# Optimization experiments

Hardware: AMD Instinct MI355X
Metric: run time of the kernel (lower is better)

## Reference

```python
import jax, jax.numpy as jnp
import numpy as np

N_ATOMS = 2_000_000
N_MOL = 50_000
NODE_DIM = 128
HIDDEN_DIM = 64


def setup_inputs() -> dict:
    key = jax.random.key(0)
    k1, k2, k3, k4, k5 = jax.random.split(key, 5)
    x_scalar = jax.random.normal(k1, (N_ATOMS, NODE_DIM), dtype=jnp.float32)
    batch = jnp.sort(jax.random.randint(k2, (N_ATOMS,), 0, N_MOL, dtype=jnp.int32))
    charge = jax.random.normal(k3, (N_MOL,), dtype=jnp.float32)
    W1 = jax.random.normal(k4, (NODE_DIM, HIDDEN_DIM), dtype=jnp.float32) / np.sqrt(NODE_DIM)
    b1 = jnp.zeros((HIDDEN_DIM,), dtype=jnp.float32)  # init.zeros_
    W2 = jax.random.normal(k5, (HIDDEN_DIM, 1), dtype=jnp.float32) / np.sqrt(HIDDEN_DIM)
    b2 = jnp.zeros((1,), dtype=jnp.float32)  # node_bias = 0.0
    return {"x_scalar": x_scalar, "batch": batch, "charge": charge,
            "W1": W1, "b1": b1, "W2": W2, "b2": b2}


def reference(x_scalar, batch, charge, W1, b1, W2, b2):
    # tiny per-atom MLP: 128 -> 64 (silu) -> 1
    h = jax.nn.silu(x_scalar @ W1 + b1)            # [N, 64]
    atom_out = (h @ W2 + b2).squeeze(-1)           # [N]
    n_mol = charge.shape[0]
    # per-molecule reductions keyed by batch
    sum_chrg = jax.ops.segment_sum(atom_out, batch, num_segments=n_mol)          # [B]
    num_atoms = jax.ops.segment_sum(jnp.ones_like(atom_out), batch, num_segments=n_mol)  # [B]
    # gather back per atom and apply total-charge correction
    tot_chrg = charge[batch]                       # [N]
    at_chrgs = atom_out + (tot_chrg - sum_chrg[batch]) / num_atoms[batch]
    return at_chrgs
```

## Files before the change

kernel.cpp:

```cpp
#include <hip/hip_runtime.h>
#include <stdint.h>

typedef __attribute__((ext_vector_type(8))) short bf16x8;
typedef __attribute__((ext_vector_type(4))) float f32x4;

__device__ inline short f2bf(float f) {
    uint32_t u = __builtin_bit_cast(uint32_t, f);
    u += 0x7FFFu + ((u >> 16) & 1u);
    return (short)(u >> 16);
}

__global__ __launch_bounds__(256) void k1_mlp(
        const float* __restrict__ X, const float* __restrict__ W1,
        const float* __restrict__ b1, const float* __restrict__ W2,
        const float* __restrict__ b2, float* __restrict__ out, int N) {
    const int lane = threadIdx.x & 63;
    const int col  = lane & 15;
    const int quad = lane >> 4;
    const int wid   = blockIdx.x * (blockDim.x >> 6) + (threadIdx.x >> 6);
    const int nwave = gridDim.x * (blockDim.x >> 6);

    bf16x8 bfrag[4][4];
#pragma unroll
    for (int nt = 0; nt < 4; ++nt)
#pragma unroll
        for (int s = 0; s < 4; ++s)
#pragma unroll
            for (int j = 0; j < 8; ++j)
                bfrag[nt][s][j] = f2bf(W1[(quad * 8 + j + 32 * s) * 64 + 16 * nt + col]);

    float b1v[4], w2v[4];
#pragma unroll
    for (int nt = 0; nt < 4; ++nt) {
        b1v[nt] = b1[16 * nt + col];
        w2v[nt] = W2[16 * nt + col];
    }
    const float b2v = b2[0];

    const int ntiles = N >> 4;
    for (int tile = wid; tile < ntiles; tile += nwave) {
        const int row0 = tile << 4;
        const float* __restrict__ xrow = X + (size_t)(row0 + col) * 128;

        f32x4 xa[4][2];
#pragma unroll
        for (int s = 0; s < 4; ++s) {
            const float* p = xrow + quad * 8 + 32 * s;
            xa[s][0] = *(const f32x4*)(p);
            xa[s][1] = *(const f32x4*)(p + 4);
        }

        f32x4 acc[4] = {{0.f,0.f,0.f,0.f},{0.f,0.f,0.f,0.f},
                        {0.f,0.f,0.f,0.f},{0.f,0.f,0.f,0.f}};
#pragma unroll
        for (int s = 0; s < 4; ++s) {
            bf16x8 afrag;
#pragma unroll
            for (int j = 0; j < 4; ++j) {
                afrag[j]     = f2bf(xa[s][0][j]);
                afrag[4 + j] = f2bf(xa[s][1][j]);
            }
#pragma unroll
            for (int nt = 0; nt < 4; ++nt)
                acc[nt] = __builtin_amdgcn_mfma_f32_16x16x32_bf16(
                              afrag, bfrag[nt][s], acc[nt], 0, 0, 0);
        }

        float p[4] = {0.f, 0.f, 0.f, 0.f};
#pragma unroll
        for (int nt = 0; nt < 4; ++nt) {
#pragma unroll
            for (int j = 0; j < 4; ++j) {
                float h  = acc[nt][j] + b1v[nt];
                float sg = 1.0f / (1.0f + __expf(-h));
                p[j] += h * sg * w2v[nt];
            }
        }
#pragma unroll
        for (int m = 1; m <= 8; m <<= 1)
#pragma unroll
            for (int j = 0; j < 4; ++j)
                p[j] += __shfl_xor(p[j], m, 64);

        if (col == 0) {
            f32x4 v = {p[0] + b2v, p[1] + b2v, p[2] + b2v, p[3] + b2v};
            *(f32x4*)(out + row0 + quad * 4) = v;
        }
    }
}

__global__ __launch_bounds__(256) void k2_seg(
        const float* __restrict__ atomout, const int* __restrict__ batch,
        const float* __restrict__ charge, float* __restrict__ corr, int N, int B) {
    int m = blockIdx.x * blockDim.x + threadIdx.x;
    if (m >= B) return;
    int lo = 0, hi = N;
    while (lo < hi) { int mid = (lo + hi) >> 1; if (batch[mid] < m) lo = mid + 1; else hi = mid; }
    int start = lo;
    lo = start; hi = N;
    while (lo < hi) { int mid = (lo + hi) >> 1; if (batch[mid] < m + 1) lo = mid + 1; else hi = mid; }
    int end = lo;
    float s = 0.f;
    for (int i = start; i < end; ++i) s += atomout[i];
    int cnt = end - start;
    corr[m] = (cnt > 0) ? (charge[m] - s) / (float)cnt : 0.f;
}

__global__ __launch_bounds__(256) void k3_apply(
        float* __restrict__ out, const int* __restrict__ batch,
        const float* __restrict__ corr, int N) {
    int i = blockIdx.x * blockDim.x + threadIdx.x;
    if (i < N) out[i] += corr[batch[i]];
}

extern "C" void kernel_launch(void* const* d_in, const int* in_sizes, int n_in,
                              void* d_out, int out_size, void* d_ws, size_t ws_size,
                              hipStream_t stream) {
    const float* X      = (const float*)d_in[0];
    const int*   batch  = (const int*)  d_in[1];
    const float* charge = (const float*)d_in[2];
    const float* W1     = (const float*)d_in[3];
    const float* b1     = (const float*)d_in[4];
    const float* W2     = (const float*)d_in[5];
    const float* b2     = (const float*)d_in[6];
    float* out  = (float*)d_out;
    float* corr = (float*)d_ws;

    const int N = in_sizes[1];
    const int B = in_sizes[2];

    k1_mlp<<<1024, 256, 0, stream>>>(X, W1, b1, W2, b2, out, N);
    k2_seg<<<(B + 255) / 256, 256, 0, stream>>>(out, batch, charge, corr, N, B);
    k3_apply<<<(N + 255) / 256, 256, 0, stream>>>(out, batch, corr, N);
}
```

Baseline: 1.351 ms.

## Coalesce X loads via swizzled LDS staging, share segment bounds, vectorize apply

The MLP kernel now loads each 16-row tile of X with fully coalesced contiguous 16-byte loads, converts to bf16, and stages it in a per-wave XOR-swizzled LDS buffer before reading MFMA A-fragments. Previously each lane read strided row segments. The segment kernel computes only one binary search per molecule and takes the end bound from the neighbouring lane with a shuffle. The apply kernel is vectorized to four atoms per thread and writes the output from a separate workspace buffer. Together these reduce uncoalesced global traffic and halve the search work, at the cost of LDS use and extra workspace memory.

```diff
diff --git a/kernel.cpp b/kernel.cpp
--- a/kernel.cpp
+++ b/kernel.cpp
@@ -2,6 +2,7 @@
 #include <stdint.h>
 
 typedef __attribute__((ext_vector_type(8))) short bf16x8;
+typedef __attribute__((ext_vector_type(4))) short bf16x4;
 typedef __attribute__((ext_vector_type(4))) float f32x4;
 
 __device__ inline short f2bf(float f) {
@@ -13,11 +14,14 @@
 __global__ __launch_bounds__(256) void k1_mlp(
         const float* __restrict__ X, const float* __restrict__ W1,
         const float* __restrict__ b1, const float* __restrict__ W2,
-        const float* __restrict__ b2, float* __restrict__ out, int N) {
+        const float* __restrict__ b2, float* __restrict__ ao, int N) {
+    __shared__ short lds[4 * 2048];
     const int lane = threadIdx.x & 63;
-    const int col  = lane & 15;
-    const int quad = lane >> 4;
-    const int wid   = blockIdx.x * (blockDim.x >> 6) + (threadIdx.x >> 6);
+    const int wv   = threadIdx.x >> 6;
+    short* wl = lds + wv * 2048;
+    const int c = lane & 15;
+    const int q = lane >> 4;
+    const int wid   = blockIdx.x * (blockDim.x >> 6) + wv;
     const int nwave = gridDim.x * (blockDim.x >> 6);
 
     bf16x8 bfrag[4][4];
@@ -27,39 +31,44 @@
         for (int s = 0; s < 4; ++s)
 #pragma unroll
             for (int j = 0; j < 8; ++j)
-                bfrag[nt][s][j] = f2bf(W1[(quad * 8 + j + 32 * s) * 64 + 16 * nt + col]);
+                bfrag[nt][s][j] = f2bf(W1[(q * 8 + j + 32 * s) * 64 + 16 * nt + c]);
 
     float b1v[4], w2v[4];
 #pragma unroll
     for (int nt = 0; nt < 4; ++nt) {
-        b1v[nt] = b1[16 * nt + col];
-        w2v[nt] = W2[16 * nt + col];
+        b1v[nt] = b1[16 * nt + c];
+        w2v[nt] = W2[16 * nt + c];
     }
     const float b2v = b2[0];
 
     const int ntiles = N >> 4;
     for (int tile = wid; tile < ntiles; tile += nwave) {
-        const int row0 = tile << 4;
-        const float* __restrict__ xrow = X + (size_t)(row0 + col) * 128;
+        const float* __restrict__ src = X + (size_t)tile * 2048;
 
-        f32x4 xa[4][2];
+        f32x4 v[8];
 #pragma unroll
-        for (int s = 0; s < 4; ++s) {
-            const float* p = xrow + quad * 8 + 32 * s;
-            xa[s][0] = *(const f32x4*)(p);
-            xa[s][1] = *(const f32x4*)(p + 4);
+        for (int k = 0; k < 8; ++k)
+            v[k] = *(const f32x4*)(src + (size_t)(k * 64 + lane) * 4);
+
+#pragma unroll
+        for (int k = 0; k < 8; ++k) {
+            int f   = k * 64 + lane;
+            int r   = f >> 5;
+            int c8  = f & 31;
+            int cc  = c8 >> 1;
+            int par = c8 & 1;
+            int idx = r * 128 + ((cc ^ (r & 7)) << 3) + (par << 2);
+            bf16x4 h;
+            h[0] = f2bf(v[k][0]); h[1] = f2bf(v[k][1]);
+            h[2] = f2bf(v[k][2]); h[3] = f2bf(v[k][3]);
+            *(bf16x4*)(wl + idx) = h;
         }
 
         f32x4 acc[4] = {{0.f,0.f,0.f,0.f},{0.f,0.f,0.f,0.f},
                         {0.f,0.f,0.f,0.f},{0.f,0.f,0.f,0.f}};
 #pragma unroll
         for (int s = 0; s < 4; ++s) {
-            bf16x8 afrag;
-#pragma unroll
-            for (int j = 0; j < 4; ++j) {
-                afrag[j]     = f2bf(xa[s][0][j]);
-                afrag[4 + j] = f2bf(xa[s][1][j]);
-            }
+            bf16x8 afrag = *(const bf16x8*)(wl + c * 128 + (((s * 4 + q) ^ (c & 7)) << 3));
 #pragma unroll
             for (int nt = 0; nt < 4; ++nt)
                 acc[nt] = __builtin_amdgcn_mfma_f32_16x16x32_bf16(
@@ -82,35 +91,51 @@
             for (int j = 0; j < 4; ++j)
                 p[j] += __shfl_xor(p[j], m, 64);
 
-        if (col == 0) {
-            f32x4 v = {p[0] + b2v, p[1] + b2v, p[2] + b2v, p[3] + b2v};
-            *(f32x4*)(out + row0 + quad * 4) = v;
+        if (c == 0) {
+            f32x4 o = {p[0] + b2v, p[1] + b2v, p[2] + b2v, p[3] + b2v};
+            *(f32x4*)(ao + (size_t)tile * 16 + q * 4) = o;
         }
     }
 }
 
+__device__ inline int lower_bound(const int* __restrict__ a, int n, int key) {
+    int lo = 0, hi = n;
+    while (lo < hi) { int mid = (lo + hi) >> 1; if (a[mid] < key) lo = mid + 1; else hi = mid; }
+    return lo;
+}
+
 __global__ __launch_bounds__(256) void k2_seg(
-        const float* __restrict__ atomout, const int* __restrict__ batch,
+        const float* __restrict__ ao, const int* __restrict__ batch,
         const float* __restrict__ charge, float* __restrict__ corr, int N, int B) {
     int m = blockIdx.x * blockDim.x + threadIdx.x;
+    int lane = threadIdx.x & 63;
+    int mc = m < B ? m : B - 1;
+    int st = lower_bound(batch, N, mc);
+    int nb = __shfl_down(st, 1, 64);
+    int en;
+    if (mc == B - 1)      en = N;
+    else if (lane == 63)  en = lower_bound(batch, N, mc + 1);
+    else                  en = nb;
     if (m >= B) return;
-    int lo = 0, hi = N;
-    while (lo < hi) { int mid = (lo + hi) >> 1; if (batch[mid] < m) lo = mid + 1; else hi = mid; }
-    int start = lo;
-    lo = start; hi = N;
-    while (lo < hi) { int mid = (lo + hi) >> 1; if (batch[mid] < m + 1) lo = mid + 1; else hi = mid; }
-    int end = lo;
     float s = 0.f;
-    for (int i = start; i < end; ++i) s += atomout[i];
-    int cnt = end - start;
+    for (int i = st; i < en; ++i) s += ao[i];
+    int cnt = en - st;
     corr[m] = (cnt > 0) ? (charge[m] - s) / (float)cnt : 0.f;
 }
 
 __global__ __launch_bounds__(256) void k3_apply(
-        float* __restrict__ out, const int* __restrict__ batch,
-        const float* __restrict__ corr, int N) {
-    int i = blockIdx.x * blockDim.x + threadIdx.x;
-    if (i < N) out[i] += corr[batch[i]];
+        float* __restrict__ out, const float* __restrict__ ao,
+        const int* __restrict__ batch, const float* __restrict__ corr, int N) {
+    int i = (blockIdx.x * blockDim.x + threadIdx.x) * 4;
+    if (i >= N) return;
+    int4  b = *(const int4*)(batch + i);
+    f32x4 a = *(const f32x4*)(ao + i);
+    f32x4 o;
+    o[0] = a[0] + corr[b.x];
+    o[1] = a[1] + corr[b.y];
+    o[2] = a[2] + corr[b.z];
+    o[3] = a[3] + corr[b.w];
+    *(f32x4*)(out + i) = o;
 }
 
 extern "C" void kernel_launch(void* const* d_in, const int* in_sizes, int n_in,
@@ -124,12 +149,14 @@
     const float* W2     = (const float*)d_in[5];
     const float* b2     = (const float*)d_in[6];
     float* out  = (float*)d_out;
-    float* corr = (float*)d_ws;
 
     const int N = in_sizes[1];
     const int B = in_sizes[2];
 
-    k1_mlp<<<1024, 256, 0, stream>>>(X, W1, b1, W2, b2, out, N);
-    k2_seg<<<(B + 255) / 256, 256, 0, stream>>>(out, batch, charge, corr, N, B);
-    k3_apply<<<(N + 255) / 256, 256, 0, stream>>>(out, batch, corr, N);
+    float* ao   = (float*)d_ws;
+    float* corr = (float*)((char*)d_ws + (size_t)N * sizeof(float));
+
+    k1_mlp<<<1024, 256, 0, stream>>>(X, W1, b1, W2, b2, ao, N);
+    k2_seg<<<(B + 255) / 256, 256, 0, stream>>>(ao, batch, charge, corr, N, B);
+    k3_apply<<<(N / 4 + 255) / 256, 256, 0, stream>>>(out, ao, batch, corr, N);
 }
```

Result: no change. 1.348 ms (-0.2%).
